# Optimization experiments

Measured on AMD Instinct MI355X. Metric: run time of the kernel, lower is better.

## Reference

```python
import jax, jax.numpy as jnp
import numpy as np

H, DK = 16, 64
D = H * DK  # d_model = 1024
B, S = 2, 2048


def setup_inputs() -> dict:
    key = jax.random.key(0)
    ks = jax.random.split(key, 11)
    std = 1.0 / np.sqrt(D)
    inp = {
        "query": jax.random.normal(ks[0], (B, S, D), dtype=jnp.float32),
        "key": jax.random.normal(ks[1], (B, S, D), dtype=jnp.float32),
        "value": jax.random.normal(ks[2], (B, S, D), dtype=jnp.float32),
        "Wq": jax.random.normal(ks[3], (D, D), dtype=jnp.float32) * std,
        "bq": jnp.zeros((D,), dtype=jnp.float32),
        "Wk": jax.random.normal(ks[4], (D, D), dtype=jnp.float32) * std,
        "bk": jnp.zeros((D,), dtype=jnp.float32),
        "Wv": jax.random.normal(ks[5], (D, D), dtype=jnp.float32) * std,
        "bv": jnp.zeros((D,), dtype=jnp.float32),
        "Wo": jax.random.normal(ks[6], (D, D), dtype=jnp.float32) * std,
        "bo": jnp.zeros((D,), dtype=jnp.float32),
    }
    return inp


def reference(query, key, value, Wq, bq, Wk, bk, Wv, bv, Wo, bo):
    # torch.nn.Linear convention: y = x @ W.T + b
    def split_heads(x):
        b, s, _ = x.shape
        return x.reshape(b, s, H, DK).transpose(0, 2, 1, 3)  # [B,H,S,DK]

    q = split_heads(query @ Wq.T + bq)
    k = split_heads(key @ Wk.T + bk)
    v = split_heads(value @ Wv.T + bv)

    scale = 1.0 / jnp.sqrt(jnp.asarray(DK, dtype=q.dtype))
    scores = jnp.einsum("bhqd,bhkd->bhqk", q, k) * scale  # [B,H,S,S]
    p_attn = jax.nn.softmax(scores, axis=-1)
    ctx = jnp.einsum("bhqk,bhkd->bhqd", p_attn, v)  # [B,H,S,DK]

    ctx = ctx.transpose(0, 2, 1, 3).reshape(query.shape[0], -1, H * DK)
    return ctx @ Wo.T + bo
```

## Files before the change

### kernel.cpp

```cpp
#include <hip/hip_runtime.h>
#include <stdint.h>

#define BATCH 2
#define SEQ   2048
#define NHEAD 16
#define DK    64
#define DMODEL 1024
#define MROWS (BATCH*SEQ)

typedef __attribute__((ext_vector_type(8))) __bf16 bf16x8;
typedef __attribute__((ext_vector_type(4))) float f32x4;
typedef __attribute__((ext_vector_type(8))) unsigned short u16x8;
typedef __attribute__((ext_vector_type(4))) unsigned short u16x4;

#define QSCALE 0.18033688f

__device__ __forceinline__ unsigned short f2bf(float f) {
  union { float f; uint32_t u; } c; c.f = f;
  uint32_t u = c.u;
  return (unsigned short)((u + 0x7fffu + ((u >> 16) & 1u)) >> 16);
}

__device__ __forceinline__ void gld16(const void* g, void* lds) {
  __builtin_amdgcn_global_load_lds(
      (const __attribute__((address_space(1))) void*)g,
      (__attribute__((address_space(3))) void*)lds,
      16, 0, 0);
}

__global__ __launch_bounds__(256)
void cvt_all(const float* __restrict__ q, const float* __restrict__ k, const float* __restrict__ v,
             const float* __restrict__ Wq, const float* __restrict__ Wk,
             const float* __restrict__ Wv, const float* __restrict__ Wo,
             unsigned short* __restrict__ Xq, unsigned short* __restrict__ Xk,
             unsigned short* __restrict__ Xv,
             unsigned short* __restrict__ Wqb, unsigned short* __restrict__ Wkb,
             unsigned short* __restrict__ Wvb, unsigned short* __restrict__ Wob) {
  int blk = blockIdx.x;
  const float* in; unsigned short* out; int base;
  if (blk < 6144) {
    int ti = blk >> 11;
    in  = (ti == 0) ? q  : (ti == 1) ? k  : v;
    out = (ti == 0) ? Xq : (ti == 1) ? Xk : Xv;
    base = (blk & 2047) * 2048;
  } else {
    int ti = (blk - 6144) >> 9;
    in  = (ti == 0) ? Wq  : (ti == 1) ? Wk  : (ti == 2) ? Wv  : Wo;
    out = (ti == 0) ? Wqb : (ti == 1) ? Wkb : (ti == 2) ? Wvb : Wob;
    base = ((blk - 6144) & 511) * 2048;
  }
  int i = base + threadIdx.x * 8;
  float4 a = *(const float4*)(in + i);
  float4 b = *(const float4*)(in + i + 4);
  u16x8 o;
  o[0]=f2bf(a.x); o[1]=f2bf(a.y); o[2]=f2bf(a.z); o[3]=f2bf(a.w);
  o[4]=f2bf(b.x); o[5]=f2bf(b.y); o[6]=f2bf(b.z); o[7]=f2bf(b.w);
  *(u16x8*)(out + i) = o;
}

__device__ __forceinline__ void gemm_body(const unsigned short* __restrict__ X,
                                          const unsigned short* __restrict__ W,
                                          const float* __restrict__ bias,
                                          unsigned short* __restrict__ Yb,
                                          float* __restrict__ Yf,
                                          int mode) {
  __shared__ unsigned short lA[128 * 64];
  __shared__ unsigned short lB[128 * 64];
  const int t = threadIdx.x;
  const int lane = t & 63, wave = t >> 6;
  const int cl = lane & 15, qd = lane >> 4;
  const int wm = wave >> 1, wn = wave & 1;
  const int rowBase = blockIdx.y * 128;
  const int colBase = blockIdx.x * 128;
  const int srow = t >> 3, sslot = t & 7;

  int aoff[2][4], boff[2][4];
  #pragma unroll
  for (int ks = 0; ks < 2; ks++)
    #pragma unroll
    for (int i = 0; i < 4; i++) {
      int ra = wm * 64 + i * 16 + cl;
      aoff[ks][i] = ra * 64 + ((ks * 4 + qd) ^ (ra & 7)) * 8;
      int rb = wn * 64 + i * 16 + cl;
      boff[ks][i] = rb * 64 + ((ks * 4 + qd) ^ (rb & 7)) * 8;
    }
  const unsigned short* xp[4];
  const unsigned short* wp[4];
  #pragma unroll
  for (int i = 0; i < 4; i++) {
    int r = i * 32 + srow;
    int chunk = sslot ^ (r & 7);
    xp[i] = X + (size_t)(rowBase + r) * DMODEL + chunk * 8;
    wp[i] = W + (size_t)(colBase + r) * DMODEL + chunk * 8;
  }

  f32x4 zero = {0.f, 0.f, 0.f, 0.f};
  f32x4 acc[4][4];
  for (int mt = 0; mt < 4; mt++) for (int nt = 0; nt < 4; nt++) acc[mt][nt] = zero;

  for (int k0 = 0; k0 < DMODEL; k0 += 64) {
    __syncthreads();
    #pragma unroll
    for (int i = 0; i < 4; i++) {
      gld16(xp[i], (char*)lA + i * 4096 + wave * 1024);
      gld16(wp[i], (char*)lB + i * 4096 + wave * 1024);
      xp[i] += 64; wp[i] += 64;
    }
    __syncthreads();
    #pragma unroll
    for (int ks = 0; ks < 2; ks++) {
      bf16x8 af[4], bfr[4];
      #pragma unroll
      for (int mt = 0; mt < 4; mt++) af[mt] = *(const bf16x8*)&lA[aoff[ks][mt]];
      #pragma unroll
      for (int nt = 0; nt < 4; nt++) bfr[nt] = *(const bf16x8*)&lB[boff[ks][nt]];
      #pragma unroll
      for (int mt = 0; mt < 4; mt++)
        #pragma unroll
        for (int nt = 0; nt < 4; nt++)
          acc[mt][nt] = __builtin_amdgcn_mfma_f32_16x16x32_bf16(af[mt], bfr[nt], acc[mt][nt], 0, 0, 0);
    }
  }
  if (mode == 2) {
    #pragma unroll
    for (int mt = 0; mt < 4; mt++) {
      int row0 = rowBase + wm * 64 + mt * 16 + qd * 4;
      int bb = row0 >> 11;
      int s_in = row0 & 2047;
      int blk = s_in & ~63;
      int n4 = (s_in & 63) >> 2;
      int l4 = n4 & 7;
      int pos = 8 * (n4 >> 3) + ((l4 < 4) ? 2 * l4 : 2 * (l4 - 4) + 1);
      #pragma unroll
      for (int nt = 0; nt < 4; nt++) {
        int c = colBase + wn * 64 + nt * 16 + cl;
        float bv = bias[c];
        int hh = c >> 6, d = c & 63;
        u16x4 v;
        #pragma unroll
        for (int r = 0; r < 4; r++) v[r] = f2bf(acc[mt][nt][r] + bv);
        *(u16x4*)&Yb[(size_t)((bb * NHEAD + hh) * 64 + d) * SEQ + blk + pos * 4] = v;
      }
    }
  } else {
    #pragma unroll
    for (int mt = 0; mt < 4; mt++) {
      int row = rowBase + wm * 64 + mt * 16 + qd * 4;
      #pragma unroll
      for (int nt = 0; nt < 4; nt++) {
        int c = colBase + wn * 64 + nt * 16 + cl;
        float bv = bias[c];
        #pragma unroll
        for (int r = 0; r < 4; r++) {
          float v = acc[mt][nt][r] + bv;
          if (mode == 3)      Yf[(size_t)(row + r) * DMODEL + c] = v;
          else if (mode == 1) Yb[(size_t)(row + r) * DMODEL + c] = f2bf(v * QSCALE);
          else                Yb[(size_t)(row + r) * DMODEL + c] = f2bf(v);
        }
      }
    }
  }
}

__global__ __launch_bounds__(256)
void gemm_qkv(const unsigned short* __restrict__ Xq, const unsigned short* __restrict__ Xk,
              const unsigned short* __restrict__ Xv,
              const unsigned short* __restrict__ Wq, const unsigned short* __restrict__ Wk,
              const unsigned short* __restrict__ Wv,
              const float* __restrict__ bq, const float* __restrict__ bk,
              const float* __restrict__ bv,
              unsigned short* __restrict__ Q, unsigned short* __restrict__ K,
              unsigned short* __restrict__ VT) {
  int z = blockIdx.z;
  const unsigned short* X = (z == 0) ? Xq : (z == 1) ? Xk : Xv;
  const unsigned short* W = (z == 0) ? Wq : (z == 1) ? Wk : Wv;
  const float* b = (z == 0) ? bq : (z == 1) ? bk : bv;
  unsigned short* Y = (z == 0) ? Q : (z == 1) ? K : VT;
  int mode = (z == 0) ? 1 : (z == 1) ? 0 : 2;
  gemm_body(X, W, b, Y, nullptr, mode);
}

__global__ __launch_bounds__(256)
void gemm_out(const unsigned short* __restrict__ CTX, const unsigned short* __restrict__ Wo,
              const float* __restrict__ bo, float* __restrict__ out) {
  gemm_body(CTX, Wo, bo, nullptr, out, 3);
}

__global__ __launch_bounds__(256)
void attn(const unsigned short* __restrict__ Q, const unsigned short* __restrict__ K,
          const unsigned short* __restrict__ VT, unsigned short* __restrict__ CTX) {
  __shared__ unsigned short lK[2 * 64 * 64];
  __shared__ unsigned short lV[2 * 64 * 64];
  const int t = threadIdx.x, lane = t & 63, wave = t >> 6;
  const int cl = lane & 15, qd = lane >> 4;
  const int qt = blockIdx.x, h = blockIdx.y, b = blockIdx.z;
  const int srow = t >> 3, sslot = t & 7;

  #pragma unroll
  for (int half = 0; half < 2; half++)
    #pragma unroll
    for (int i = 0; i < 2; i++) {
      int r = i * 32 + srow;
      int chunk = sslot ^ (r & 7);
      gld16(Q + (size_t)(b * SEQ + qt * 128 + half * 64 + r) * DMODEL + h * 64 + chunk * 8,
            (char*)lK + half * 8192 + i * 4096 + wave * 1024);
    }
  __syncthreads();
  bf16x8 qf[2][2];
  #pragma unroll
  for (int qg = 0; qg < 2; qg++)
    #pragma unroll
    for (int ks = 0; ks < 2; ks++) {
      int r = wave * 16 + cl;
      int slot = (ks * 4 + qd) ^ (r & 7);
      qf[qg][ks] = *(const bf16x8*)&lK[qg * 4096 + r * 64 + slot * 8];
    }
  __syncthreads();

  int ka[8], va[8];
  #pragma unroll
  for (int ks = 0; ks < 2; ks++)
    #pragma unroll
    for (int nt = 0; nt < 4; nt++) {
      int rk = nt * 16 + cl;
      ka[ks * 4 + nt] = rk * 64 + ((ks * 4 + qd) ^ (rk & 7)) * 8;
    }
  #pragma unroll
  for (int ntp = 0; ntp < 2; ntp++)
    #pragma unroll
    for (int dt = 0; dt < 4; dt++) {
      int d = dt * 16 + cl;
      va[ntp * 4 + dt] = d * 64 + ((4 * ntp + qd) ^ (d & 7)) * 8;
    }

  const unsigned short* kp[2];
  const unsigned short* vp[2];
  #pragma unroll
  for (int i = 0; i < 2; i++) {
    int r = i * 32 + srow;
    int chunk = sslot ^ (r & 7);
    kp[i] = K + (size_t)(b * SEQ + r) * DMODEL + h * 64 + chunk * 8;
    vp[i] = VT + (size_t)((b * NHEAD + h) * 64 + r) * SEQ + chunk * 8;
    gld16(kp[i], (char*)lK + i * 4096 + wave * 1024);
    gld16(vp[i], (char*)lV + i * 4096 + wave * 1024);
    kp[i] += 64 * DMODEL; vp[i] += 64;
  }

  f32x4 zero = {0.f, 0.f, 0.f, 0.f};
  f32x4 o[2][4];
  f32x4 osum[2];
  #pragma unroll
  for (int qg = 0; qg < 2; qg++) {
    #pragma unroll
    for (int dt = 0; dt < 4; dt++) o[qg][dt] = zero;
    osum[qg] = zero;
  }
  bf16x8 ones;
  #pragma unroll
  for (int j = 0; j < 8; j++) ones[j] = (__bf16)1.0f;

  #pragma unroll 2
  for (int kt = 0; kt < SEQ / 64; kt++) {
    const int cb = (kt & 1) * 4096;
    __syncthreads();
    if (kt + 1 < SEQ / 64) {
      const int nb = ((kt + 1) & 1) * 8192;
      #pragma unroll
      for (int i = 0; i < 2; i++) {
        gld16(kp[i], (char*)lK + nb + i * 4096 + wave * 1024);
        gld16(vp[i], (char*)lV + nb + i * 4096 + wave * 1024);
        kp[i] += 64 * DMODEL; vp[i] += 64;
      }
    }

    f32x4 sc[2][4];
    #pragma unroll
    for (int qg = 0; qg < 2; qg++)
      #pragma unroll
      for (int nt = 0; nt < 4; nt++) sc[qg][nt] = zero;
    #pragma unroll
    for (int ks = 0; ks < 2; ks++)
      #pragma unroll
      for (int nt = 0; nt < 4; nt++) {
        bf16x8 kf = *(const bf16x8*)&lK[cb + ka[ks * 4 + nt]];
        sc[0][nt] = __builtin_amdgcn_mfma_f32_16x16x32_bf16(kf, qf[0][ks], sc[0][nt], 0, 0, 0);
        sc[1][nt] = __builtin_amdgcn_mfma_f32_16x16x32_bf16(kf, qf[1][ks], sc[1][nt], 0, 0, 0);
      }

    bf16x8 pb[2][2];
    #pragma unroll
    for (int qg = 0; qg < 2; qg++)
      #pragma unroll
      for (int ntp = 0; ntp < 2; ntp++) {
        bf16x8 x;
        #pragma unroll
        for (int j = 0; j < 4; j++)
          x[j] = (__bf16)__builtin_amdgcn_exp2f(sc[qg][2 * ntp][j]);
        #pragma unroll
        for (int j = 0; j < 4; j++)
          x[4 + j] = (__bf16)__builtin_amdgcn_exp2f(sc[qg][2 * ntp + 1][j]);
        pb[qg][ntp] = x;
      }

    #pragma unroll
    for (int qg = 0; qg < 2; qg++) {
      osum[qg] = __builtin_amdgcn_mfma_f32_16x16x32_bf16(ones, pb[qg][0], osum[qg], 0, 0, 0);
      osum[qg] = __builtin_amdgcn_mfma_f32_16x16x32_bf16(ones, pb[qg][1], osum[qg], 0, 0, 0);
    }

    #pragma unroll
    for (int ntp = 0; ntp < 2; ntp++)
      #pragma unroll
      for (int dt = 0; dt < 4; dt++) {
        bf16x8 vf = *(const bf16x8*)&lV[cb + va[ntp * 4 + dt]];
        o[0][dt] = __builtin_amdgcn_mfma_f32_16x16x32_bf16(vf, pb[0][ntp], o[0][dt], 0, 0, 0);
        o[1][dt] = __builtin_amdgcn_mfma_f32_16x16x32_bf16(vf, pb[1][ntp], o[1][dt], 0, 0, 0);
      }
  }

  #pragma unroll
  for (int qg = 0; qg < 2; qg++) {
    float inv = 1.f / osum[qg][0];
    int row = b * SEQ + qt * 128 + qg * 64 + wave * 16 + cl;
    #pragma unroll
    for (int dt = 0; dt < 4; dt++) {
      u16x4 v;
      #pragma unroll
      for (int r = 0; r < 4; r++) v[r] = f2bf(o[qg][dt][r] * inv);
      *(u16x4*)&CTX[(size_t)row * DMODEL + h * 64 + dt * 16 + qd * 4] = v;
    }
  }
}

extern "C" void kernel_launch(void* const* d_in, const int* in_sizes, int n_in,
                              void* d_out, int out_size, void* d_ws, size_t ws_size,
                              hipStream_t stream) {
  const float* q  = (const float*)d_in[0];
  const float* k  = (const float*)d_in[1];
  const float* v  = (const float*)d_in[2];
  const float* Wq = (const float*)d_in[3]; const float* bq = (const float*)d_in[4];
  const float* Wk = (const float*)d_in[5]; const float* bk = (const float*)d_in[6];
  const float* Wv = (const float*)d_in[7]; const float* bv = (const float*)d_in[8];
  const float* Wo = (const float*)d_in[9]; const float* bo = (const float*)d_in[10];
  float* out = (float*)d_out;

  char* ws = (char*)d_ws;
  const size_t MB = 1u << 20;
  unsigned short* Xq  = (unsigned short*)(ws + 0 * MB);
  unsigned short* Xk  = (unsigned short*)(ws + 8 * MB);
  unsigned short* Xv  = (unsigned short*)(ws + 16 * MB);
  unsigned short* Wqb = (unsigned short*)(ws + 24 * MB);
  unsigned short* Wkb = (unsigned short*)(ws + 26 * MB);
  unsigned short* Wvb = (unsigned short*)(ws + 28 * MB);
  unsigned short* Wob = (unsigned short*)(ws + 70 * MB);
  unsigned short* Qp  = (unsigned short*)(ws + 32 * MB);
  unsigned short* Kp  = (unsigned short*)(ws + 40 * MB);
  unsigned short* VT  = (unsigned short*)(ws + 48 * MB);
  unsigned short* CTX = (unsigned short*)(ws + 56 * MB);

  cvt_all<<<8192, 256, 0, stream>>>(q, k, v, Wq, Wk, Wv, Wo,
                                    Xq, Xk, Xv, Wqb, Wkb, Wvb, Wob);

  gemm_qkv<<<dim3(DMODEL / 128, MROWS / 128, 3), 256, 0, stream>>>(
      Xq, Xk, Xv, Wqb, Wkb, Wvb, bq, bk, bv, Qp, Kp, VT);

  attn<<<dim3(SEQ / 128, NHEAD, BATCH), 256, 0, stream>>>(Qp, Kp, VT, CTX);

  gemm_out<<<dim3(DMODEL / 128, MROWS / 128), 256, 0, stream>>>(CTX, Wob, bo, out);
}
```

Before: 223.9 us.

## Template GEMM modes, swap MFMA operands for vector stores, remap block order

The GEMM body becomes a template over its output mode, which removes runtime branching. For the non-transposed outputs, the MFMA operand order is swapped so each lane holds four consecutive columns, so the epilogue can issue vectorized float4 and u16x4 stores with a vector bias load instead of scalar strided stores. Block indices for the GEMMs are remapped so consecutive blocks walk down M sharing a weight column tile, and attention blocks are permuted across heads and batches, likely to spread work across XCDs and caches. The remapping relies on hardcoded grid sizes.

Result: slower. 233.8 us (+4.4%).

```diff
diff --git a/kernel.cpp b/kernel.cpp
--- a/kernel.cpp
+++ b/kernel.cpp
@@ -58,20 +58,19 @@
   *(u16x8*)(out + i) = o;
 }
 
+template <int MODE>
 __device__ __forceinline__ void gemm_body(const unsigned short* __restrict__ X,
                                           const unsigned short* __restrict__ W,
                                           const float* __restrict__ bias,
                                           unsigned short* __restrict__ Yb,
                                           float* __restrict__ Yf,
-                                          int mode) {
+                                          int rowBase, int colBase) {
   __shared__ unsigned short lA[128 * 64];
   __shared__ unsigned short lB[128 * 64];
   const int t = threadIdx.x;
   const int lane = t & 63, wave = t >> 6;
   const int cl = lane & 15, qd = lane >> 4;
   const int wm = wave >> 1, wn = wave & 1;
-  const int rowBase = blockIdx.y * 128;
-  const int colBase = blockIdx.x * 128;
   const int srow = t >> 3, sslot = t & 7;
 
   int aoff[2][4], boff[2][4];
@@ -117,11 +116,16 @@
       #pragma unroll
       for (int mt = 0; mt < 4; mt++)
         #pragma unroll
-        for (int nt = 0; nt < 4; nt++)
-          acc[mt][nt] = __builtin_amdgcn_mfma_f32_16x16x32_bf16(af[mt], bfr[nt], acc[mt][nt], 0, 0, 0);
-    }
-  }
-  if (mode == 2) {
+        for (int nt = 0; nt < 4; nt++) {
+          if (MODE == 2)
+            acc[mt][nt] = __builtin_amdgcn_mfma_f32_16x16x32_bf16(af[mt], bfr[nt], acc[mt][nt], 0, 0, 0);
+          else
+            acc[mt][nt] = __builtin_amdgcn_mfma_f32_16x16x32_bf16(bfr[nt], af[mt], acc[mt][nt], 0, 0, 0);
+        }
+    }
+  }
+
+  if (MODE == 2) {
     #pragma unroll
     for (int mt = 0; mt < 4; mt++) {
       int row0 = rowBase + wm * 64 + mt * 16 + qd * 4;
@@ -144,18 +148,25 @@
     }
   } else {
     #pragma unroll
-    for (int mt = 0; mt < 4; mt++) {
-      int row = rowBase + wm * 64 + mt * 16 + qd * 4;
-      #pragma unroll
-      for (int nt = 0; nt < 4; nt++) {
-        int c = colBase + wn * 64 + nt * 16 + cl;
-        float bv = bias[c];
-        #pragma unroll
-        for (int r = 0; r < 4; r++) {
-          float v = acc[mt][nt][r] + bv;
-          if (mode == 3)      Yf[(size_t)(row + r) * DMODEL + c] = v;
-          else if (mode == 1) Yb[(size_t)(row + r) * DMODEL + c] = f2bf(v * QSCALE);
-          else                Yb[(size_t)(row + r) * DMODEL + c] = f2bf(v);
+    for (int nt = 0; nt < 4; nt++) {
+      int col = colBase + wn * 64 + nt * 16 + qd * 4;
+      f32x4 bv4 = *(const f32x4*)&bias[col];
+      #pragma unroll
+      for (int mt = 0; mt < 4; mt++) {
+        int row = rowBase + wm * 64 + mt * 16 + cl;
+        if (MODE == 3) {
+          f32x4 v;
+          #pragma unroll
+          for (int r = 0; r < 4; r++) v[r] = acc[mt][nt][r] + bv4[r];
+          *(f32x4*)&Yf[(size_t)row * DMODEL + col] = v;
+        } else {
+          u16x4 v;
+          #pragma unroll
+          for (int r = 0; r < 4; r++) {
+            float x = acc[mt][nt][r] + bv4[r];
+            v[r] = f2bf(MODE == 1 ? x * QSCALE : x);
+          }
+          *(u16x4*)&Yb[(size_t)row * DMODEL + col] = v;
         }
       }
     }
@@ -171,19 +182,20 @@
               const float* __restrict__ bv,
               unsigned short* __restrict__ Q, unsigned short* __restrict__ K,
               unsigned short* __restrict__ VT) {
+  int id = blockIdx.x;
+  int by = id & 31, bx = id >> 5;
   int z = blockIdx.z;
-  const unsigned short* X = (z == 0) ? Xq : (z == 1) ? Xk : Xv;
-  const unsigned short* W = (z == 0) ? Wq : (z == 1) ? Wk : Wv;
-  const float* b = (z == 0) ? bq : (z == 1) ? bk : bv;
-  unsigned short* Y = (z == 0) ? Q : (z == 1) ? K : VT;
-  int mode = (z == 0) ? 1 : (z == 1) ? 0 : 2;
-  gemm_body(X, W, b, Y, nullptr, mode);
+  if (z == 0)      gemm_body<1>(Xq, Wq, bq, Q,  nullptr, by * 128, bx * 128);
+  else if (z == 1) gemm_body<0>(Xk, Wk, bk, K,  nullptr, by * 128, bx * 128);
+  else             gemm_body<2>(Xv, Wv, bv, VT, nullptr, by * 128, bx * 128);
 }
 
 __global__ __launch_bounds__(256)
 void gemm_out(const unsigned short* __restrict__ CTX, const unsigned short* __restrict__ Wo,
               const float* __restrict__ bo, float* __restrict__ out) {
-  gemm_body(CTX, Wo, bo, nullptr, out, 3);
+  int id = blockIdx.x;
+  int by = id & 31, bx = id >> 5;
+  gemm_body<3>(CTX, Wo, bo, nullptr, out, by * 128, bx * 128);
 }
 
 __global__ __launch_bounds__(256)
@@ -193,7 +205,10 @@
   __shared__ unsigned short lV[2 * 64 * 64];
   const int t = threadIdx.x, lane = t & 63, wave = t >> 6;
   const int cl = lane & 15, qd = lane >> 4;
-  const int qt = blockIdx.x, h = blockIdx.y, b = blockIdx.z;
+  const int flat = blockIdx.x + 16 * blockIdx.y + 256 * blockIdx.z;
+  const int loc = flat >> 3;
+  const int p = (flat & 7) * 4 + (loc >> 4);
+  const int qt = loc & 15, h = p & 15, b = p >> 4;
   const int srow = t >> 3, sslot = t & 7;
 
   #pragma unroll
@@ -361,10 +376,10 @@
   cvt_all<<<8192, 256, 0, stream>>>(q, k, v, Wq, Wk, Wv, Wo,
                                     Xq, Xk, Xv, Wqb, Wkb, Wvb, Wob);
 
-  gemm_qkv<<<dim3(DMODEL / 128, MROWS / 128, 3), 256, 0, stream>>>(
+  gemm_qkv<<<dim3(256, 1, 3), 256, 0, stream>>>(
       Xq, Xk, Xv, Wqb, Wkb, Wvb, bq, bk, bv, Qp, Kp, VT);
 
   attn<<<dim3(SEQ / 128, NHEAD, BATCH), 256, 0, stream>>>(Qp, Kp, VT, CTX);
 
-  gemm_out<<<dim3(DMODEL / 128, MROWS / 128), 256, 0, stream>>>(CTX, Wob, bo, out);
-}
+  gemm_out<<<256, 256, 0, stream>>>(CTX, Wob, bo, out);
+}
```
